# Performance work log

Measured on AMD Instinct MI355X. Metric: run time of the kernel, lower is better.

## Reference

```python
import jax, jax.numpy as jnp
import numpy as np


def setup_inputs() -> dict:
    key = jax.random.key(0)
    k1, k2 = jax.random.split(key)
    pred = jax.random.normal(k1, (4, 8192, 3), dtype=jnp.float32)
    target = jax.random.normal(k2, (4, 8192, 3), dtype=jnp.float32)
    return {"pred": pred, "target": target}


def reference(pred, target):
    # Pairwise squared distances via the expansion ||p-q||^2 = ||p||^2 + ||q||^2 - 2 p.q
    # Avoids materializing the O(B*M*N*3) diff tensor of the naive broadcast.
    p_sq = jnp.sum(pred * pred, axis=-1)          # [B, M]
    q_sq = jnp.sum(target * target, axis=-1)      # [B, N]
    cross = jnp.einsum("bmd,bnd->bmn", pred, target)  # [B, M, N]
    dist_sq = p_sq[:, :, None] + q_sq[:, None, :] - 2.0 * cross  # [B, M, N]
    min_dist_pred = jnp.min(dist_sq, axis=2).mean(axis=1)    # [B] min over target per pred point
    min_dist_target = jnp.min(dist_sq, axis=1).mean(axis=1)  # [B] min over pred per target point
    return jnp.mean(min_dist_pred + min_dist_target)
```

## Files before the change

kernel.cpp:

```cpp
#include <hip/hip_runtime.h>


#define THREADS 512
#define P 8
#define S 32
#define G 128
#define TILE 64
#define LSTRIDE (TILE + 1)

typedef float float2_t __attribute__((ext_vector_type(2)));
typedef float float4_t __attribute__((ext_vector_type(4)));

static __device__ __forceinline__ float2_t pk_fma_bl_bh(float2_t a, float2_t b) {
  float2_t d;
  asm("v_pk_fma_f32 %0, %1, %2, %2 op_sel:[0,0,1] op_sel_hi:[1,0,1]"
      : "=v"(d) : "v"(a), "v"(b));
  return d;
}
static __device__ __forceinline__ float2_t pk_fma_bh(float2_t a, float2_t b, float2_t c) {
  float2_t d;
  asm("v_pk_fma_f32 %0, %1, %2, %3 op_sel:[0,1,0] op_sel_hi:[1,1,1]"
      : "=v"(d) : "v"(a), "v"(b), "v"(c));
  return d;
}
static __device__ __forceinline__ float2_t pk_fma_bl(float2_t a, float2_t b, float2_t c) {
  float2_t d;
  asm("v_pk_fma_f32 %0, %1, %2, %3 op_sel:[0,0,0] op_sel_hi:[1,0,1]"
      : "=v"(d) : "v"(a), "v"(b), "v"(c));
  return d;
}

__global__ __launch_bounds__(THREADS, 4) void chamfer_min_kernel(
    const float* __restrict__ pred, const float* __restrict__ target,
    float* __restrict__ out, int M, float scale) {
  const int blocksPerDir = M / G;
  int pblk = blockIdx.x % blocksPerDir;
  int bd = blockIdx.x / blocksPerDir;
  int dir = bd & 1;
  int b = bd >> 1;
  const float* src = (dir ? target : pred) + (size_t)b * M * 3;
  const float* ref = (dir ? pred : target) + (size_t)b * M * 3;

  __shared__ float4_t lds[S * LSTRIDE];

  int t = threadIdx.x;
  int g = t >> 4;
  int l = t & 15;

  float cm[P];
  float2_t a2x[P / 2], a2y[P / 2], a2z[P / 2];
  int pbase = pblk * G;
#pragma unroll
  for (int i = 0; i < P / 2; ++i) {
    int p0 = pbase + l + 16 * (2 * i);
    int p1 = pbase + l + 16 * (2 * i + 1);
    float x0 = src[p0 * 3 + 0], y0 = src[p0 * 3 + 1], z0 = src[p0 * 3 + 2];
    float x1 = src[p1 * 3 + 0], y1 = src[p1 * 3 + 1], z1 = src[p1 * 3 + 2];
    cm[2 * i] = x0 * x0 + y0 * y0 + z0 * z0;
    cm[2 * i + 1] = x1 * x1 + y1 * y1 + z1 * z1;
    a2x[i] = (float2_t){-2.f * x0, -2.f * x1};
    a2y[i] = (float2_t){-2.f * y0, -2.f * y1};
    a2z[i] = (float2_t){-2.f * z0, -2.f * z1};
  }
  float mlo[P / 2], mhi[P / 2];
#pragma unroll
  for (int i = 0; i < P / 2; ++i) { mlo[i] = 3.0e38f; mhi[i] = 3.0e38f; }

  const int sliceLen = M / S;
  const int ntiles = sliceLen / TILE;
  for (int k = 0; k < ntiles; ++k) {
    __syncthreads();
#pragma unroll
    for (int i = 0; i < (S * TILE) / THREADS; ++i) {
      int idx = t + THREADS * i;
      int s = idx >> 6;
      int jj = idx & (TILE - 1);
      int n = s * sliceLen + k * TILE + jj;
      float qx = ref[n * 3 + 0], qy = ref[n * 3 + 1], qz = ref[n * 3 + 2];
      lds[s * LSTRIDE + jj] =
          (float4_t){qx, qy, qz, qx * qx + qy * qy + qz * qz};
    }
    __syncthreads();
    const float4_t* tp = lds + g * LSTRIDE;
#pragma unroll 2
    for (int j = 0; j < TILE; j += 4) {
      float4_t q0 = tp[j + 0];
      float4_t q1 = tp[j + 1];
      float4_t q2 = tp[j + 2];
      float4_t q3 = tp[j + 3];
      float2_t q0xy = __builtin_shufflevector(q0, q0, 0, 1);
      float2_t q0zw = __builtin_shufflevector(q0, q0, 2, 3);
      float2_t q1xy = __builtin_shufflevector(q1, q1, 0, 1);
      float2_t q1zw = __builtin_shufflevector(q1, q1, 2, 3);
      float2_t q2xy = __builtin_shufflevector(q2, q2, 0, 1);
      float2_t q2zw = __builtin_shufflevector(q2, q2, 2, 3);
      float2_t q3xy = __builtin_shufflevector(q3, q3, 0, 1);
      float2_t q3zw = __builtin_shufflevector(q3, q3, 2, 3);
#pragma unroll
      for (int i = 0; i < P / 2; ++i) {
        float2_t d0 = pk_fma_bl(a2x[i], q0xy,
                        pk_fma_bh(a2y[i], q0xy, pk_fma_bl_bh(a2z[i], q0zw)));
        float2_t d1 = pk_fma_bl(a2x[i], q1xy,
                        pk_fma_bh(a2y[i], q1xy, pk_fma_bl_bh(a2z[i], q1zw)));
        float2_t d2 = pk_fma_bl(a2x[i], q2xy,
                        pk_fma_bh(a2y[i], q2xy, pk_fma_bl_bh(a2z[i], q2zw)));
        float2_t d3 = pk_fma_bl(a2x[i], q3xy,
                        pk_fma_bh(a2y[i], q3xy, pk_fma_bl_bh(a2z[i], q3zw)));
        mlo[i] = fminf(fminf(mlo[i], d0.x), d1.x);
        mlo[i] = fminf(fminf(mlo[i], d2.x), d3.x);
        mhi[i] = fminf(fminf(mhi[i], d0.y), d1.y);
        mhi[i] = fminf(fminf(mhi[i], d2.y), d3.y);
      }
    }
  }

  __syncthreads();
  float* lmin = (float*)lds;
  float* lcm = (float*)lds + S * G;
#pragma unroll
  for (int i = 0; i < P / 2; ++i) {
    lmin[g * G + (l + 16 * (2 * i))] = mlo[i];
    lmin[g * G + (l + 16 * (2 * i + 1))] = mhi[i];
    if (g == 0) {
      lcm[l + 16 * (2 * i)] = cm[2 * i];
      lcm[l + 16 * (2 * i + 1)] = cm[2 * i + 1];
    }
  }
  __syncthreads();
  float v = 0.f;
  if (t < G) {
    float mn = 3.0e38f;
#pragma unroll
    for (int s = 0; s < S; ++s) mn = fminf(mn, lmin[s * G + t]);
    v = lcm[t] + mn;
  }
  for (int off = 32; off > 0; off >>= 1) v += __shfl_down(v, off, 64);
  __shared__ float ws[THREADS / 64];
  if ((t & 63) == 0) ws[t >> 6] = v;
  __syncthreads();
  if (t == 0) {
    float bsum = 0.f;
#pragma unroll
    for (int w = 0; w < THREADS / 64; ++w) bsum += ws[w];
    atomicAdd(out, bsum * scale);
  }
}

extern "C" void kernel_launch(void* const* d_in, const int* in_sizes, int n_in,
                              void* d_out, int out_size, void* d_ws,
                              size_t ws_size, hipStream_t stream) {
  const float* pred = (const float*)d_in[0];
  const float* target = (const float*)d_in[1];
  float* out = (float*)d_out;
  const int B = 4;
  const int M = in_sizes[0] / (B * 3);

  float scale = 1.0f / (float)(B * M);

  hipMemsetAsync(out, 0, sizeof(float), stream);
  int blocks = B * 2 * (M / G);
  chamfer_min_kernel<<<blocks, THREADS, 0, stream>>>(pred, target, out, M,
                                                     scale);
}
```

Baseline: 96.96 us.

## Split target range across blocks and reduce partial minima in second kernel

Each block now processes only half of the reference points (TSPLIT=2), doubling the grid so more waves are resident per CU to hide latency. Per-point partial minima go to a workspace buffer, and a separate reduction kernel takes the min over splits and sums in double precision. The launch bound is also raised to 8 blocks per CU. This costs an extra kernel launch and workspace traffic, and may cause register pressure under the tighter launch bound.

```diff
diff --git a/kernel.cpp b/kernel.cpp
--- a/kernel.cpp
+++ b/kernel.cpp
@@ -7,6 +7,7 @@
 #define G 128
 #define TILE 64
 #define LSTRIDE (TILE + 1)
+#define TSPLIT 2
 
 typedef float float2_t __attribute__((ext_vector_type(2)));
 typedef float float4_t __attribute__((ext_vector_type(4)));
@@ -30,12 +31,15 @@
   return d;
 }
 
-__global__ __launch_bounds__(THREADS, 4) void chamfer_min_kernel(
+__global__ __launch_bounds__(THREADS, 8) void chamfer_min_kernel(
     const float* __restrict__ pred, const float* __restrict__ target,
-    float* __restrict__ out, int M, float scale) {
+    float* __restrict__ wsmin, int M) {
   const int blocksPerDir = M / G;
-  int pblk = blockIdx.x % blocksPerDir;
-  int bd = blockIdx.x / blocksPerDir;
+  int bid = blockIdx.x;
+  int pblk = bid % blocksPerDir;
+  int rest = bid / blocksPerDir;
+  int ts = rest % TSPLIT;
+  int bd = rest / TSPLIT;
   int dir = bd & 1;
   int b = bd >> 1;
   const float* src = (dir ? target : pred) + (size_t)b * M * 3;
@@ -66,7 +70,9 @@
 #pragma unroll
   for (int i = 0; i < P / 2; ++i) { mlo[i] = 3.0e38f; mhi[i] = 3.0e38f; }
 
-  const int sliceLen = M / S;
+  const int spanLen = M / TSPLIT;
+  const int tbase = ts * spanLen;
+  const int sliceLen = spanLen / S;
   const int ntiles = sliceLen / TILE;
   for (int k = 0; k < ntiles; ++k) {
     __syncthreads();
@@ -75,7 +81,7 @@
       int idx = t + THREADS * i;
       int s = idx >> 6;
       int jj = idx & (TILE - 1);
-      int n = s * sliceLen + k * TILE + jj;
+      int n = tbase + s * sliceLen + k * TILE + jj;
       float qx = ref[n * 3 + 0], qy = ref[n * 3 + 1], qz = ref[n * 3 + 2];
       lds[s * LSTRIDE + jj] =
           (float4_t){qx, qy, qz, qx * qx + qy * qy + qz * qz};
@@ -127,22 +133,35 @@
     }
   }
   __syncthreads();
-  float v = 0.f;
   if (t < G) {
     float mn = 3.0e38f;
 #pragma unroll
     for (int s = 0; s < S; ++s) mn = fminf(mn, lmin[s * G + t]);
-    v = lcm[t] + mn;
+    int pid = (b * 2 + dir) * M + pbase + t;
+    wsmin[(size_t)pid * TSPLIT + ts] = lcm[t] + mn;
   }
-  for (int off = 32; off > 0; off >>= 1) v += __shfl_down(v, off, 64);
-  __shared__ float ws[THREADS / 64];
-  if ((t & 63) == 0) ws[t >> 6] = v;
+}
+
+__global__ __launch_bounds__(256) void chamfer_reduce_kernel(
+    const float* __restrict__ wsmin, float* __restrict__ out, int npts,
+    float scale) {
+  int tid = blockIdx.x * blockDim.x + threadIdx.x;
+  int stride = gridDim.x * blockDim.x;
+  double acc = 0.0;
+  for (int p = tid; p < npts; p += stride) {
+    float2_t v = ((const float2_t*)wsmin)[p];
+    acc += (double)fminf(v.x, v.y);
+  }
+  for (int off = 32; off > 0; off >>= 1) acc += __shfl_down(acc, off, 64);
+  __shared__ double wsum[256 / 64];
+  int t = threadIdx.x;
+  if ((t & 63) == 0) wsum[t >> 6] = acc;
   __syncthreads();
   if (t == 0) {
-    float bsum = 0.f;
+    double s = 0.0;
 #pragma unroll
-    for (int w = 0; w < THREADS / 64; ++w) bsum += ws[w];
-    atomicAdd(out, bsum * scale);
+    for (int w = 0; w < 256 / 64; ++w) s += wsum[w];
+    atomicAdd(out, (float)(s * (double)scale));
   }
 }
 
@@ -152,13 +171,15 @@
   const float* pred = (const float*)d_in[0];
   const float* target = (const float*)d_in[1];
   float* out = (float*)d_out;
+  float* wsmin = (float*)d_ws;
   const int B = 4;
   const int M = in_sizes[0] / (B * 3);
 
   float scale = 1.0f / (float)(B * M);
 
   hipMemsetAsync(out, 0, sizeof(float), stream);
-  int blocks = B * 2 * (M / G);
-  chamfer_min_kernel<<<blocks, THREADS, 0, stream>>>(pred, target, out, M,
-                                                     scale);
+  int blocks = B * 2 * (M / G) * TSPLIT;
+  chamfer_min_kernel<<<blocks, THREADS, 0, stream>>>(pred, target, wsmin, M);
+  int npts = B * 2 * M;
+  chamfer_reduce_kernel<<<64, 256, 0, stream>>>(wsmin, out, npts, scale);
 }
```

Result: slower. 109.0 us (+12.5%).
